# Kernel tuning notes

Hardware: AMD Instinct MI355X
Metric: run time of the kernel (lower is better)

Reference implementation:

```python
import jax, jax.numpy as jnp
import numpy as np

N_CELLS, N_GENES = 10000, 4000
CELL_F, GENE_F = 2000, 50
HID, LAT, NCLUST = 256, 64, 20
N_EDGES = 640000
ALPHA = 1.0


def _lin(key, fan_in, fan_out):
    k1, k2 = jax.random.split(key)
    bound = 1.0 / np.sqrt(fan_in)
    w = jax.random.uniform(k1, (fan_in, fan_out), jnp.float32, -bound, bound)
    b = jax.random.uniform(k2, (fan_out,), jnp.float32, -bound, bound)
    return w, b


def setup_inputs() -> dict:
    key = jax.random.key(0)
    ks = jax.random.split(key, 20)
    inp = {
        'cell_x': jax.random.normal(ks[0], (N_CELLS, CELL_F), jnp.float32),
        'gene_x': jax.random.normal(ks[1], (N_GENES, GENE_F), jnp.float32),
        'edge_row': jax.random.randint(ks[2], (N_EDGES,), 0, N_CELLS),
        'edge_col': jax.random.randint(ks[3], (N_EDGES,), 0, N_GENES),
        'edge_val': jax.random.uniform(ks[4], (N_EDGES,), jnp.float32),
    }
    # layer 0: cell_in=CELL_F, gene_in=GENE_F -> HID
    inp['l0_cs_w'], inp['l0_cs_b'] = _lin(ks[5], CELL_F, HID)
    inp['l0_cn_w'], inp['l0_cn_b'] = _lin(ks[6], GENE_F, HID)
    inp['l0_gs_w'], inp['l0_gs_b'] = _lin(ks[7], GENE_F, HID)
    inp['l0_gn_w'], inp['l0_gn_b'] = _lin(ks[8], CELL_F, HID)
    # layer 1: HID -> HID
    inp['l1_cs_w'], inp['l1_cs_b'] = _lin(ks[9], HID, HID)
    inp['l1_cn_w'], inp['l1_cn_b'] = _lin(ks[10], HID, HID)
    inp['l1_gs_w'], inp['l1_gs_b'] = _lin(ks[11], HID, HID)
    inp['l1_gn_w'], inp['l1_gn_b'] = _lin(ks[12], HID, HID)
    # latent heads and decoders
    inp['cl_w'], inp['cl_b'] = _lin(ks[13], HID, LAT)
    inp['gl_w'], inp['gl_b'] = _lin(ks[14], HID, LAT)
    inp['cd_w'], inp['cd_b'] = _lin(ks[15], LAT, N_GENES)
    inp['gd_w'], inp['gd_b'] = _lin(ks[16], LAT, N_CELLS)
    inp['centers'] = jax.random.normal(ks[17], (NCLUST, LAT), jnp.float32)
    return inp


def _bip_conv(cell_x, gene_x, er, ec, ev,
              cs_w, cs_b, cn_w, cn_b, gs_w, gs_b, gn_w, gn_b):
    # sparse adjacency matmul as gather + segment_sum over edge list
    cell_neigh = jax.ops.segment_sum(ev[:, None] * gene_x[ec], er,
                                     num_segments=cell_x.shape[0])
    gene_neigh = jax.ops.segment_sum(ev[:, None] * cell_x[er], ec,
                                     num_segments=gene_x.shape[0])
    cell_out = jax.nn.relu(cell_x @ cs_w + cs_b + cell_neigh @ cn_w + cn_b)
    gene_out = jax.nn.relu(gene_x @ gs_w + gs_b + gene_neigh @ gn_w + gn_b)
    return cell_out, gene_out


def reference(cell_x, gene_x, edge_row, edge_col, edge_val,
              l0_cs_w, l0_cs_b, l0_cn_w, l0_cn_b, l0_gs_w, l0_gs_b, l0_gn_w, l0_gn_b,
              l1_cs_w, l1_cs_b, l1_cn_w, l1_cn_b, l1_gs_w, l1_gs_b, l1_gn_w, l1_gn_b,
              cl_w, cl_b, gl_w, gl_b, cd_w, cd_b, gd_w, gd_b, centers):
    c, g = _bip_conv(cell_x, gene_x, edge_row, edge_col, edge_val,
                     l0_cs_w, l0_cs_b, l0_cn_w, l0_cn_b,
                     l0_gs_w, l0_gs_b, l0_gn_w, l0_gn_b)
    c, g = _bip_conv(c, g, edge_row, edge_col, edge_val,
                     l1_cs_w, l1_cs_b, l1_cn_w, l1_cn_b,
                     l1_gs_w, l1_gs_b, l1_gn_w, l1_gn_b)
    z_cells = c @ cl_w + cl_b
    z_genes = g @ gl_w + gl_b
    cell_recon = z_cells @ cd_w + cd_b
    gene_recon = z_genes @ gd_w + gd_b
    # Student-t cluster assignment (DEC)
    sq_dist = jnp.sum((z_cells[:, None, :] - centers[None, :, :]) ** 2, axis=-1)
    numerator = (1.0 + sq_dist / ALPHA) ** (-(ALPHA + 1.0) / 2.0)
    q = numerator / jnp.sum(numerator, axis=1, keepdims=True)
    return z_cells, z_genes, cell_recon, gene_recon, q
```

## Files before the change

### kernel.cpp

```cpp
#include <hip/hip_runtime.h>

#define N_CELLS 10000
#define N_GENES 4000
#define CELL_F  2000
#define CELL_FP 2048
#define GENE_F  50
#define GENE_FP 64
#define HID     256
#define LAT     64
#define NCLUST  20
#define N_EDGES 640000

typedef __attribute__((ext_vector_type(8))) short    bf16x8;
typedef __attribute__((ext_vector_type(8))) unsigned short u16x8;
typedef __attribute__((ext_vector_type(4))) float    f32x4;

__device__ __forceinline__ unsigned short f2bf(float f) {
    unsigned int u = __float_as_uint(f);
    unsigned int r = (u + 0x7FFFu + ((u >> 16) & 1u)) >> 16;
    return (unsigned short)r;
}
__device__ __forceinline__ float bf2f(unsigned short h) {
    return __uint_as_float(((unsigned int)h) << 16);
}

#define GLOAD_LDS16(gp, lp) __builtin_amdgcn_global_load_lds( \
    (const __attribute__((address_space(1))) void*)(gp), \
    (__attribute__((address_space(3))) void*)(lp), 16, 0, 0)

struct GemmDesc {
    const unsigned short *A, *BT;
    const float *bias;
    float *C;
    unsigned short *Cbf;
    int M, N, K;
    int gx, nwg, blk0;
};
struct GemmArgs2 { GemmDesc d[2]; };
struct ScatArgs {
    const int *er, *ec; const float *ev;
    int *cur_c, *cur_g;
    int *ci; float *cv; int *gi; float *gv;
};

template<int TM, bool BIAS, bool WF32, bool WBF, bool TEPI, bool QTAIL, bool SCAT>
__global__ __launch_bounds__(256)
void gemm_multi(GemmArgs2 ga, int gemm0, int qstart,
                const float* __restrict__ zq, const float* __restrict__ cent,
                float* __restrict__ qout, ScatArgs sa)
{
    constexpr int SMEM = (TM * 128 + 8192) > 16640 ? (TM * 128 + 8192) : 16640;
    __shared__ __align__(16) unsigned char smem[SMEM];
    unsigned short* As = (unsigned short*)smem;
    unsigned short* Bs = As + TM * 64;

    if (SCAT && (int)blockIdx.x < gemm0) {
        int e = blockIdx.x * 256 + threadIdx.x;
        int r = sa.er[e], c = sa.ec[e];
        float v = sa.ev[e];
        int pc = atomicAdd(&sa.cur_c[r], 1);
        sa.ci[pc] = c; sa.cv[pc] = v;
        int pg = atomicAdd(&sa.cur_g[c], 1);
        sa.gi[pg] = r; sa.gv[pg] = v;
        return;
    }

    if (QTAIL && (int)blockIdx.x >= qstart) {
        float* cs = (float*)smem;
        int tid = threadIdx.x;
        for (int l = tid; l < NCLUST * LAT; l += 256) cs[l] = cent[l];
        __syncthreads();
        int c = (blockIdx.x - qstart) * 256 + tid;
        if (c >= N_CELLS) return;
        float zr[LAT];
        #pragma unroll
        for (int k = 0; k < LAT; ++k) zr[k] = zq[(size_t)c * LAT + k];
        float num[NCLUST];
        float denom = 0.0f;
        for (int j = 0; j < NCLUST; ++j) {
            float d = 0.0f;
            #pragma unroll
            for (int k = 0; k < LAT; ++k) {
                float t = zr[k] - cs[j * LAT + k];
                d += t * t;
            }
            float n = 1.0f / (1.0f + d);
            num[j] = n;
            denom += n;
        }
        float inv = 1.0f / denom;
        for (int j = 0; j < NCLUST; ++j) qout[(size_t)c * NCLUST + j] = num[j] * inv;
        return;
    }

    int b = blockIdx.x;
    int p = (b >= ga.d[1].blk0) ? 1 : 0;
    const GemmDesc d = ga.d[p];
    int lin = b - d.blk0;
    int q8 = d.nwg >> 3, r8 = d.nwg & 7;
    int xcd = lin & 7, idx = lin >> 3;
    int wgid = (xcd < r8 ? xcd * (q8 + 1) : r8 * (q8 + 1) + (xcd - r8) * q8) + idx;
    int by = wgid / d.gx;
    int bx = wgid - by * d.gx;

    const int tid  = threadIdx.x;
    const int lane = tid & 63;
    const int w    = tid >> 6;
    const int cn   = lane & 15;
    const int rj   = lane >> 4;
    const int row0 = by * TM;
    const int col0 = bx * 64;

    constexpr int AI = TM / 32;
    constexpr int MF = TM / 64;

    size_t arow[AI];
    unsigned short* ldsA[AI];
    #pragma unroll
    for (int j = 0; j < AI; ++j) {
        int slot = (w * AI + j) * 64 + lane;
        int rs = slot >> 3, ss = slot & 7, cs = ss ^ (rs & 7);
        arow[j] = (size_t)min(row0 + rs, d.M - 1) * d.K + cs * 8;
        ldsA[j] = As + (w * AI + j) * 512;
    }
    const int sb0 = (w * 2) * 64 + lane;
    const int sb1 = sb0 + 64;
    const int rb0 = sb0 >> 3, cb0 = (sb0 & 7) ^ (rb0 & 7);
    const int rb1 = sb1 >> 3, cb1 = (sb1 & 7) ^ (rb1 & 7);
    const size_t brow0 = (size_t)(col0 + rb0) * d.K + cb0 * 8;
    const size_t brow1 = (size_t)(col0 + rb1) * d.K + cb1 * 8;
    unsigned short* ldsB = Bs + (w * 2) * 512;

    int aoff0[MF], aoff1[MF];
    #pragma unroll
    for (int mf = 0; mf < MF; ++mf) {
        int rA = w * (TM / 4) + mf * 16 + cn, swA = rA & 7, abase = rA * 64;
        aoff0[mf] = abase + ((rj)     ^ swA) * 8;
        aoff1[mf] = abase + ((rj + 4) ^ swA) * 8;
    }

    f32x4 acc[MF][4] = {};

    for (int kt = 0; kt < d.K; kt += 64) {
        #pragma unroll
        for (int j = 0; j < AI; ++j) GLOAD_LDS16(d.A + arow[j] + kt, ldsA[j]);
        GLOAD_LDS16(d.BT + brow0 + kt, ldsB);
        GLOAD_LDS16(d.BT + brow1 + kt, ldsB + 512);
        __syncthreads();
        bf16x8 a0[MF], a1[MF];
        #pragma unroll
        for (int mf = 0; mf < MF; ++mf) {
            a0[mf] = *(const bf16x8*)&As[aoff0[mf]];
            a1[mf] = *(const bf16x8*)&As[aoff1[mf]];
        }
        #pragma unroll
        for (int f = 0; f < 4; ++f) {
            int rB = f * 16 + cn, swB = rB & 7, bb = rB * 64;
            bf16x8 b0 = *(const bf16x8*)&Bs[bb + ((rj)     ^ swB) * 8];
            bf16x8 b1 = *(const bf16x8*)&Bs[bb + ((rj + 4) ^ swB) * 8];
            #pragma unroll
            for (int mf = 0; mf < MF; ++mf) {
                acc[mf][f] = __builtin_amdgcn_mfma_f32_16x16x32_bf16(a0[mf], b0, acc[mf][f], 0, 0, 0);
                acc[mf][f] = __builtin_amdgcn_mfma_f32_16x16x32_bf16(a1[mf], b1, acc[mf][f], 0, 0, 0);
            }
        }
        __syncthreads();
    }

    if (TEPI) {
        float* Cs = (float*)smem;
        __syncthreads();
        #pragma unroll
        for (int f = 0; f < 4; ++f)
            #pragma unroll
            for (int j = 0; j < 4; ++j)
                Cs[(w * 16 + rj * 4 + j) * 65 + f * 16 + cn] = acc[0][f][j];
        __syncthreads();
        #pragma unroll
        for (int i = 0; i < 4; ++i) {
            int slot = tid + i * 256;
            int rr = slot >> 4, c4 = (slot & 15) * 4;
            int gr = row0 + rr, gc = col0 + c4;
            if (gr < d.M && gc < d.N) {
                const float* cp = &Cs[rr * 65 + c4];
                float4 bv = BIAS ? *(const float4*)&d.bias[gc] : float4{0, 0, 0, 0};
                float4 v;
                v.x = cp[0] + bv.x; v.y = cp[1] + bv.y;
                v.z = cp[2] + bv.z; v.w = cp[3] + bv.w;
                *(float4*)&d.C[(size_t)gr * d.N + gc] = v;
            }
        }
    } else {
        #pragma unroll
        for (int mf = 0; mf < MF; ++mf) {
            #pragma unroll
            for (int f = 0; f < 4; ++f) {
                int col = col0 + f * 16 + cn;
                if (col >= d.N) continue;
                float bv = BIAS ? d.bias[col] : 0.0f;
                #pragma unroll
                for (int j = 0; j < 4; ++j) {
                    int r = row0 + w * (TM / 4) + mf * 16 + rj * 4 + j;
                    if (r < d.M) {
                        float val = acc[mf][f][j] + bv;
                        if (WF32) d.C[(size_t)r * d.N + col] = val;
                        if (WBF)  d.Cbf[(size_t)r * d.N + col] = f2bf(val);
                    }
                }
            }
        }
    }
}

struct PackDesc {
    const float* W1; const float* W2; unsigned short* BT;
    int Kr, Kp, N1, N2, Np, xb, blk0;
};
struct PackArgs { PackDesc d[8]; };

#define CNT_BLK   2500
#define CVTC_BLK  10000
#define CVTG_BLK  125
#define PACK_BLK0 (CNT_BLK + CVTC_BLK + CVTG_BLK)

__global__ __launch_bounds__(256)
void prep_kernel(const int* __restrict__ er, const int* __restrict__ ec,
                 int* __restrict__ cnt_c, int* __restrict__ cnt_g,
                 const float* __restrict__ cell_x, unsigned short* __restrict__ cellx_bf,
                 const float* __restrict__ gene_x, unsigned short* __restrict__ genex_bf,
                 PackArgs pa)
{
    __shared__ float tile[32][33];
    int b = blockIdx.x;
    int tid = threadIdx.x;
    if (b < CNT_BLK) {
        int e = b * 256 + tid;
        atomicAdd(&cnt_c[er[e]], 1);
        atomicAdd(&cnt_g[ec[e]], 1);
        return;
    }
    if (b < CNT_BLK + CVTC_BLK) {
        int row = b - CNT_BLK;
        int col = tid * 8;
        u16x8 v = {0, 0, 0, 0, 0, 0, 0, 0};
        if (col < CELL_F) {
            const float* src = cell_x + (size_t)row * CELL_F + col;
            float4 f0 = *(const float4*)src;
            float4 f1 = *(const float4*)(src + 4);
            v[0] = f2bf(f0.x); v[1] = f2bf(f0.y); v[2] = f2bf(f0.z); v[3] = f2bf(f0.w);
            v[4] = f2bf(f1.x); v[5] = f2bf(f1.y); v[6] = f2bf(f1.z); v[7] = f2bf(f1.w);
        }
        ((u16x8*)(cellx_bf + (size_t)row * CELL_FP))[tid] = v;
        return;
    }
    if (b < PACK_BLK0) {
        int idx = (b - CNT_BLK - CVTC_BLK) * 256 + tid;
        int row = idx >> 3, c8 = idx & 7;
        int col = c8 * 8;
        u16x8 v = {0, 0, 0, 0, 0, 0, 0, 0};
        #pragma unroll
        for (int j = 0; j < 8; ++j)
            if (col + j < GENE_F) v[j] = f2bf(gene_x[(size_t)row * GENE_F + col + j]);
        ((u16x8*)(genex_bf + (size_t)row * GENE_FP))[c8] = v;
        return;
    }
    int pb = b;
    int p = 0;
    #pragma unroll
    for (int i = 1; i < 8; ++i) if (pb >= pa.d[i].blk0) p = i;
    const PackDesc d = pa.d[p];
    int local = pb - d.blk0;
    int kb = local % d.xb, nb = local / d.xb;
    int k0 = kb * 32, n0 = nb * 32;
    int tx = tid & 31, ty = tid >> 5;
    #pragma unroll
    for (int yy = 0; yy < 4; ++yy) {
        int k = k0 + ty + yy * 8;
        int n = n0 + tx;
        float v = 0.0f;
        if (k < d.Kr) {
            if (n < d.N1) v = d.W1[(size_t)k * d.N1 + n];
            else if (n < d.N1 + d.N2) v = d.W2[(size_t)k * d.N2 + (n - d.N1)];
        }
        tile[ty + yy * 8][tx] = v;
    }
    __syncthreads();
    #pragma unroll
    for (int yy = 0; yy < 4; ++yy) {
        int n = n0 + ty + yy * 8;
        int k = k0 + tx;
        if (n < d.Np)
            d.BT[(size_t)n * d.Kp + k] = f2bf(tile[tx][ty + yy * 8]);
    }
}

__global__ __launch_bounds__(1024)
void scan2_kernel(const int* __restrict__ cnt_c, int* __restrict__ ptr_c, int* __restrict__ cur_c,
                  const int* __restrict__ cnt_g, int* __restrict__ ptr_g, int* __restrict__ cur_g)
{
    const int* cnt = blockIdx.x ? cnt_g : cnt_c;
    int* ptr = blockIdx.x ? ptr_g : ptr_c;
    int* cur = blockIdx.x ? cur_g : cur_c;
    int  n   = blockIdx.x ? N_GENES : N_CELLS;
    __shared__ int part[1024];
    int t = threadIdx.x;
    int chunk = (n + 1023) / 1024;
    int lo = t * chunk, hi = min(lo + chunk, n);
    int s = 0;
    for (int i = lo; i < hi; ++i) s += cnt[i];
    part[t] = s;
    __syncthreads();
    #pragma unroll
    for (int off = 1; off < 1024; off <<= 1) {
        int v = (t >= off) ? part[t - off] : 0;
        __syncthreads();
        part[t] += v;
        __syncthreads();
    }
    if (t == 1023) ptr[n] = part[1023];
    int run = part[t] - s;
    for (int i = lo; i < hi; ++i) { ptr[i] = run; cur[i] = run; run += cnt[i]; }
}

struct AggSide {
    const int *ptr, *nbr; const float *val;
    const unsigned short *src, *pre;
    const float *b1, *b2;
    unsigned short *out;
};
struct AggArgs { AggSide s[2]; };

__global__ __launch_bounds__(256)
void agg2_kernel(AggArgs aa)
{
    __shared__ __align__(16) float red[4][256];
    int b = blockIdx.x;
    int side = (b >= N_CELLS) ? 1 : 0;
    const AggSide S = aa.s[side];
    int r = side ? b - N_CELLS : b;
    int t = threadIdx.x;
    int w = t >> 6;
    int lane = t & 63;
    int s = S.ptr[r], e = S.ptr[r + 1];
    int n = e - s;
    int chunk = (n + 3) >> 2;
    int ws = s + w * chunk;
    int we = min(ws + chunk, e);
    const ushort4* src4 = (const ushort4*)S.src;
    float4 acc = {0.0f, 0.0f, 0.0f, 0.0f};
    for (int base = ws; base < we; base += 16) {
        int   nb = 0;
        float vb = 0.0f;
        if (lane < 16 && base + lane < we) {
            nb = S.nbr[base + lane];
            vb = S.val[base + lane];
        }
        #pragma unroll
        for (int j = 0; j < 16; ++j) {
            int   jj = __shfl(nb, j);
            float vv = __shfl(vb, j);
            ushort4 a = src4[(size_t)jj * 128 + 64 + lane];
            acc.x += vv * bf2f(a.x);
            acc.y += vv * bf2f(a.y);
            acc.z += vv * bf2f(a.z);
            acc.w += vv * bf2f(a.w);
        }
    }
    *(float4*)&red[w][lane * 4] = acc;
    __syncthreads();
    float x = red[0][t] + red[1][t] + red[2][t] + red[3][t]
            + bf2f(S.pre[(size_t)r * 512 + t]) + S.b1[t] + S.b2[t];
    S.out[(size_t)r * 256 + t] = f2bf(fmaxf(x, 0.0f));
}

extern "C" void kernel_launch(void* const* d_in, const int* in_sizes, int n_in,
                              void* d_out, int out_size, void* d_ws, size_t ws_size,
                              hipStream_t stream)
{
    const float* cell_x  = (const float*)d_in[0];
    const float* gene_x  = (const float*)d_in[1];
    const int*   er      = (const int*)d_in[2];
    const int*   ec      = (const int*)d_in[3];
    const float* ev      = (const float*)d_in[4];
    const float* l0_cs_w = (const float*)d_in[5];  const float* l0_cs_b = (const float*)d_in[6];
    const float* l0_cn_w = (const float*)d_in[7];  const float* l0_cn_b = (const float*)d_in[8];
    const float* l0_gs_w = (const float*)d_in[9];  const float* l0_gs_b = (const float*)d_in[10];
    const float* l0_gn_w = (const float*)d_in[11]; const float* l0_gn_b = (const float*)d_in[12];
    const float* l1_cs_w = (const float*)d_in[13]; const float* l1_cs_b = (const float*)d_in[14];
    const float* l1_cn_w = (const float*)d_in[15]; const float* l1_cn_b = (const float*)d_in[16];
    const float* l1_gs_w = (const float*)d_in[17]; const float* l1_gs_b = (const float*)d_in[18];
    const float* l1_gn_w = (const float*)d_in[19]; const float* l1_gn_b = (const float*)d_in[20];
    const float* cl_w = (const float*)d_in[21]; const float* cl_b = (const float*)d_in[22];
    const float* gl_w = (const float*)d_in[23]; const float* gl_b = (const float*)d_in[24];
    const float* cd_w = (const float*)d_in[25]; const float* cd_b = (const float*)d_in[26];
    const float* gd_w = (const float*)d_in[27]; const float* gd_b = (const float*)d_in[28];
    const float* centers = (const float*)d_in[29];

    float* out = (float*)d_out;
    float* z_cells    = out;
    float* z_genes    = out + 640000;
    float* cell_recon = out + 896000;
    float* gene_recon = out + 40896000;
    float* q          = out + 80896000;

    char* wsp = (char*)d_ws;
    auto alloc = [&](size_t bytes) -> void* {
        void* p = (void*)wsp;
        wsp += (bytes + 255) & ~(size_t)255;
        return p;
    };
    unsigned short* pre_c_bf = (unsigned short*)alloc((size_t)N_CELLS * 512 * 2);
    unsigned short* pre_g_bf = (unsigned short*)alloc((size_t)N_GENES * 512 * 2);
    unsigned short* c1_bf    = (unsigned short*)alloc((size_t)N_CELLS * 256 * 2);
    unsigned short* g1_bf    = (unsigned short*)alloc((size_t)N_GENES * 256 * 2);
    unsigned short* c2_bf    = (unsigned short*)alloc((size_t)N_CELLS * 256 * 2);
    unsigned short* g2_bf    = (unsigned short*)alloc((size_t)N_GENES * 256 * 2);
    unsigned short* zc_bf    = (unsigned short*)alloc((size_t)N_CELLS * 64 * 2);
    unsigned short* zg_bf    = (unsigned short*)alloc((size_t)N_GENES * 64 * 2);
    unsigned short* cellx_bf = (unsigned short*)alloc((size_t)N_CELLS * CELL_FP * 2);
    unsigned short* genex_bf = (unsigned short*)alloc((size_t)N_GENES * GENE_FP * 2);
    unsigned short* W0cT = (unsigned short*)alloc((size_t)512 * CELL_FP * 2);
    unsigned short* W0gT = (unsigned short*)alloc((size_t)512 * GENE_FP * 2);
    unsigned short* W1cT = (unsigned short*)alloc((size_t)512 * HID * 2);
    unsigned short* W1gT = (unsigned short*)alloc((size_t)512 * HID * 2);
    unsigned short* WzcT = (unsigned short*)alloc((size_t)64 * HID * 2);
    unsigned short* WzgT = (unsigned short*)alloc((size_t)64 * HID * 2);
    unsigned short* WdcT = (unsigned short*)alloc((size_t)4032 * 64 * 2);
    unsigned short* WdgT = (unsigned short*)alloc((size_t)10048 * 64 * 2);
    int* cnt_c = (int*)alloc((size_t)(N_CELLS + N_GENES) * 4);
    int* cnt_g = cnt_c + N_CELLS;
    int* ptr_c = (int*)alloc((size_t)(N_CELLS + 1) * 4);
    int* ptr_g = (int*)alloc((size_t)(N_GENES + 1) * 4);
    int* cur_c = (int*)alloc((size_t)N_CELLS * 4);
    int* cur_g = (int*)alloc((size_t)N_GENES * 4);
    int*   ci = (int*)alloc((size_t)N_EDGES * 4);
    float* cv = (float*)alloc((size_t)N_EDGES * 4);
    int*   gi = (int*)alloc((size_t)N_EDGES * 4);
    float* gv = (float*)alloc((size_t)N_EDGES * 4);

    hipMemsetAsync(cnt_c, 0, (size_t)(N_CELLS + N_GENES) * 4, stream);

    {
        PackArgs pa;
        auto set = [&](int i, const float* W1, const float* W2, unsigned short* BT,
                       int Kr, int Kp, int N1, int N2, int Np, int blk0) -> int {
            int xb = Kp / 32, yb = Np / 32;
            pa.d[i] = {W1, W2, BT, Kr, Kp, N1, N2, Np, xb, blk0};
            return blk0 + xb * yb;
        };
        int nb = PACK_BLK0;
        nb = set(0, l0_cs_w, l0_gn_w, W0cT, CELL_F, CELL_FP, HID, HID, 512, nb);
        nb = set(1, l0_gs_w, l0_cn_w, W0gT, GENE_F, GENE_FP, HID, HID, 512, nb);
        nb = set(2, l1_cs_w, l1_gn_w, W1cT, HID, HID, HID, HID, 512, nb);
        nb = set(3, l1_gs_w, l1_cn_w, W1gT, HID, HID, HID, HID, 512, nb);
        nb = set(4, cl_w, nullptr, WzcT, HID, HID, LAT, 0, 64, nb);
        nb = set(5, gl_w, nullptr, WzgT, HID, HID, LAT, 0, 64, nb);
        nb = set(6, cd_w, nullptr, WdcT, LAT, LAT, N_GENES, 0, 4032, nb);
        nb = set(7, gd_w, nullptr, WdgT, LAT, LAT, N_CELLS, 0, 10048, nb);
        prep_kernel<<<nb, 256, 0, stream>>>(er, ec, cnt_c, cnt_g,
                                            cell_x, cellx_bf, gene_x, genex_bf, pa);
    }

    scan2_kernel<<<2, 1024, 0, stream>>>(cnt_c, ptr_c, cur_c, cnt_g, ptr_g, cur_g);

    auto mkdesc = [](const unsigned short* A, const unsigned short* BT, const float* bias,
                     float* C, unsigned short* Cbf, int M, int N, int K, int TMv,
                     int blk0) -> GemmDesc {
        int gx = (N + 63) / 64, gy = (M + TMv - 1) / TMv;
        return {A, BT, bias, C, Cbf, M, N, K, gx, gx * gy, blk0};
    };
    ScatArgs sa0 = {er, ec, ev, cur_c, cur_g, ci, cv, gi, gv};
    ScatArgs saN = {};

    {
        GemmArgs2 ga;
        ga.d[0] = mkdesc(cellx_bf, W0cT, nullptr, nullptr, pre_c_bf, N_CELLS, 512, CELL_FP, 128, CNT_BLK);
        ga.d[1] = mkdesc(genex_bf, W0gT, nullptr, nullptr, pre_g_bf, N_GENES, 512, GENE_FP, 128,
                         CNT_BLK + ga.d[0].nwg);
        gemm_multi<128, false, false, true, false, false, true>
            <<<ga.d[1].blk0 + ga.d[1].nwg, 256, 0, stream>>>(
            ga, CNT_BLK, 1 << 30, nullptr, nullptr, nullptr, sa0);
    }

    {
        AggArgs aa;
        aa.s[0] = {ptr_c, ci, cv, pre_g_bf, pre_c_bf, l0_cs_b, l0_cn_b, c1_bf};
        aa.s[1] = {ptr_g, gi, gv, pre_c_bf, pre_g_bf, l0_gs_b, l0_gn_b, g1_bf};
        agg2_kernel<<<N_CELLS + N_GENES, 256, 0, stream>>>(aa);
    }

    {
        GemmArgs2 ga;
        ga.d[0] = mkdesc(c1_bf, W1cT, nullptr, nullptr, pre_c_bf, N_CELLS, 512, HID, 128, 0);
        ga.d[1] = mkdesc(g1_bf, W1gT, nullptr, nullptr, pre_g_bf, N_GENES, 512, HID, 128,
                         ga.d[0].nwg);
        gemm_multi<128, false, false, true, false, false, false>
            <<<ga.d[1].blk0 + ga.d[1].nwg, 256, 0, stream>>>(
            ga, 0, 1 << 30, nullptr, nullptr, nullptr, saN);
    }

    {
        AggArgs aa;
        aa.s[0] = {ptr_c, ci, cv, pre_g_bf, pre_c_bf, l1_cs_b, l1_cn_b, c2_bf};
        aa.s[1] = {ptr_g, gi, gv, pre_c_bf, pre_g_bf, l1_gs_b, l1_gn_b, g2_bf};
        agg2_kernel<<<N_CELLS + N_GENES, 256, 0, stream>>>(aa);
    }

    {
        GemmArgs2 ga;
        ga.d[0] = mkdesc(c2_bf, WzcT, cl_b, z_cells, zc_bf, N_CELLS, LAT, HID, 64, 0);
        ga.d[1] = mkdesc(g2_bf, WzgT, gl_b, z_genes, zg_bf, N_GENES, LAT, HID, 64, ga.d[0].nwg);
        gemm_multi<64, true, true, true, false, false, false>
            <<<ga.d[1].blk0 + ga.d[1].nwg, 256, 0, stream>>>(
            ga, 0, 1 << 30, nullptr, nullptr, nullptr, saN);
    }

    {
        GemmArgs2 ga;
        ga.d[0] = mkdesc(zc_bf, WdcT, cd_b, cell_recon, nullptr, N_CELLS, N_GENES, LAT, 64, 0);
        ga.d[1] = mkdesc(zg_bf, WdgT, gd_b, gene_recon, nullptr, N_GENES, N_CELLS, LAT, 64,
                         ga.d[0].nwg);
        int qstart = ga.d[1].blk0 + ga.d[1].nwg;
        int qblocks = (N_CELLS + 255) / 256;
        gemm_multi<64, true, true, false, true, true, false>
            <<<qstart + qblocks, 256, 0, stream>>>(
            ga, 0, qstart, z_cells, centers, q, saN);
    }
}
```

Measured before the change: 480.2 us.

## Gather raw gene features into cell rows and fuse layer-0 cell aggregation into GEMM

Layer 0's cell-neighbor term is reassociated: the sparse sum of raw 50-wide gene features is gathered into an extra K-segment of the padded cell input, and the l0_cn weights are appended to the packed cell weight. This lets one big GEMM produce the final relu'd cell output with both biases, and drops the 256-wide cell-side aggregation pass for layer 0. The gene side only computes its self term from gene features, and the cell GEMM's second half supplies the gene-neighbor projection. The cost is a larger K (2112), one extra gather kernel, and an extra launch that serialises the first GEMM stage.

```diff
diff --git a/kernel.cpp b/kernel.cpp
--- a/kernel.cpp
+++ b/kernel.cpp
@@ -3,7 +3,7 @@
 #define N_CELLS 10000
 #define N_GENES 4000
 #define CELL_F  2000
-#define CELL_FP 2048
+#define CELL_FX 2112
 #define GENE_F  50
 #define GENE_FP 64
 #define HID     256
@@ -35,6 +35,8 @@
     unsigned short *Cbf;
     int M, N, K;
     int gx, nwg, blk0;
+    const float *bias2;
+    unsigned short *Cbf2;
 };
 struct GemmArgs2 { GemmDesc d[2]; };
 struct ScatArgs {
@@ -43,7 +45,7 @@
     int *ci; float *cv; int *gi; float *gv;
 };
 
-template<int TM, bool BIAS, bool WF32, bool WBF, bool TEPI, bool QTAIL, bool SCAT>
+template<int TM, bool BIAS, bool WF32, bool WBF, bool TEPI, bool QTAIL, bool SCAT, bool RSPLIT>
 __global__ __launch_bounds__(256)
 void gemm_multi(GemmArgs2 ga, int gemm0, int qstart,
                 const float* __restrict__ zq, const float* __restrict__ cent,
@@ -188,6 +190,27 @@
                 v.x = cp[0] + bv.x; v.y = cp[1] + bv.y;
                 v.z = cp[2] + bv.z; v.w = cp[3] + bv.w;
                 *(float4*)&d.C[(size_t)gr * d.N + gc] = v;
+            }
+        }
+    } else if (RSPLIT) {
+        #pragma unroll
+        for (int mf = 0; mf < MF; ++mf) {
+            #pragma unroll
+            for (int f = 0; f < 4; ++f) {
+                int col = col0 + f * 16 + cn;
+                #pragma unroll
+                for (int j = 0; j < 4; ++j) {
+                    int r = row0 + w * (TM / 4) + mf * 16 + rj * 4 + j;
+                    if (r < d.M) {
+                        float val = acc[mf][f][j];
+                        if (col < 256) {
+                            val += d.bias[col] + d.bias2[col];
+                            d.Cbf[(size_t)r * 256 + col] = f2bf(fmaxf(val, 0.0f));
+                        } else {
+                            d.Cbf2[(size_t)r * 256 + (col - 256)] = f2bf(val);
+                        }
+                    }
+                }
             }
         }
     } else {
@@ -212,8 +235,46 @@
     }
 }
 
+__global__ __launch_bounds__(256)
+void rawgather_kernel(const int* __restrict__ ptr, const int* __restrict__ nbr,
+                      const float* __restrict__ val,
+                      const unsigned short* __restrict__ gx,
+                      unsigned short* __restrict__ cellx)
+{
+    int w = threadIdx.x >> 6, lane = threadIdx.x & 63;
+    int r = blockIdx.x * 4 + w;
+    int s = ptr[r], e = ptr[r + 1];
+    int g = lane >> 4, sub = lane & 15;
+    const ushort4* gx4 = (const ushort4*)gx;
+    float4 acc = {0.0f, 0.0f, 0.0f, 0.0f};
+    for (int base = s; base < e; base += 16) {
+        int nb = 0; float vb = 0.0f;
+        if (lane < 16 && base + lane < e) { nb = nbr[base + lane]; vb = val[base + lane]; }
+        #pragma unroll
+        for (int jj = 0; jj < 4; ++jj) {
+            int ei = jj * 4 + g;
+            int j  = __shfl(nb, ei);
+            float v = __shfl(vb, ei);
+            ushort4 a = gx4[(size_t)j * 16 + sub];
+            acc.x += v * bf2f(a.x);
+            acc.y += v * bf2f(a.y);
+            acc.z += v * bf2f(a.z);
+            acc.w += v * bf2f(a.w);
+        }
+    }
+    acc.x += __shfl_xor(acc.x, 16); acc.x += __shfl_xor(acc.x, 32);
+    acc.y += __shfl_xor(acc.y, 16); acc.y += __shfl_xor(acc.y, 32);
+    acc.z += __shfl_xor(acc.z, 16); acc.z += __shfl_xor(acc.z, 32);
+    acc.w += __shfl_xor(acc.w, 16); acc.w += __shfl_xor(acc.w, 32);
+    if (lane < 16) {
+        ushort4 o;
+        o.x = f2bf(acc.x); o.y = f2bf(acc.y); o.z = f2bf(acc.z); o.w = f2bf(acc.w);
+        ((ushort4*)(cellx + (size_t)r * CELL_FX + 2048))[sub] = o;
+    }
+}
+
 struct PackDesc {
-    const float* W1; const float* W2; unsigned short* BT;
+    const float* W1; const float* W2; const float* W3; unsigned short* BT;
     int Kr, Kp, N1, N2, Np, xb, blk0;
 };
 struct PackArgs { PackDesc d[8]; };
@@ -250,7 +311,7 @@
             v[0] = f2bf(f0.x); v[1] = f2bf(f0.y); v[2] = f2bf(f0.z); v[3] = f2bf(f0.w);
             v[4] = f2bf(f1.x); v[5] = f2bf(f1.y); v[6] = f2bf(f1.z); v[7] = f2bf(f1.w);
         }
-        ((u16x8*)(cellx_bf + (size_t)row * CELL_FP))[tid] = v;
+        ((u16x8*)(cellx_bf + (size_t)row * CELL_FX))[tid] = v;
         return;
     }
     if (b < PACK_BLK0) {
@@ -281,6 +342,9 @@
         if (k < d.Kr) {
             if (n < d.N1) v = d.W1[(size_t)k * d.N1 + n];
             else if (n < d.N1 + d.N2) v = d.W2[(size_t)k * d.N2 + (n - d.N1)];
+        } else if (d.W3 && k >= 2048) {
+            int kk = k - 2048;
+            if (kk < GENE_F && n < HID) v = d.W3[(size_t)kk * HID + n];
         }
         tile[ty + yy * 8][tx] = v;
     }
@@ -327,17 +391,18 @@
     const unsigned short *src, *pre;
     const float *b1, *b2;
     unsigned short *out;
+    int srcRow4, srcOff4, preRow;
 };
-struct AggArgs { AggSide s[2]; };
+struct AggArgs { AggSide s[2]; int nc; };
 
 __global__ __launch_bounds__(256)
 void agg2_kernel(AggArgs aa)
 {
     __shared__ __align__(16) float red[4][256];
     int b = blockIdx.x;
-    int side = (b >= N_CELLS) ? 1 : 0;
+    int side = (b >= aa.nc) ? 1 : 0;
     const AggSide S = aa.s[side];
-    int r = side ? b - N_CELLS : b;
+    int r = side ? b - aa.nc : b;
     int t = threadIdx.x;
     int w = t >> 6;
     int lane = t & 63;
@@ -359,7 +424,7 @@
         for (int j = 0; j < 16; ++j) {
             int   jj = __shfl(nb, j);
             float vv = __shfl(vb, j);
-            ushort4 a = src4[(size_t)jj * 128 + 64 + lane];
+            ushort4 a = src4[(size_t)jj * S.srcRow4 + S.srcOff4 + lane];
             acc.x += vv * bf2f(a.x);
             acc.y += vv * bf2f(a.y);
             acc.z += vv * bf2f(a.z);
@@ -369,7 +434,7 @@
     *(float4*)&red[w][lane * 4] = acc;
     __syncthreads();
     float x = red[0][t] + red[1][t] + red[2][t] + red[3][t]
-            + bf2f(S.pre[(size_t)r * 512 + t]) + S.b1[t] + S.b2[t];
+            + bf2f(S.pre[(size_t)r * S.preRow + t]) + S.b1[t] + S.b2[t];
     S.out[(size_t)r * 256 + t] = f2bf(fmaxf(x, 0.0f));
 }
 
@@ -417,10 +482,10 @@
     unsigned short* g2_bf    = (unsigned short*)alloc((size_t)N_GENES * 256 * 2);
     unsigned short* zc_bf    = (unsigned short*)alloc((size_t)N_CELLS * 64 * 2);
     unsigned short* zg_bf    = (unsigned short*)alloc((size_t)N_GENES * 64 * 2);
-    unsigned short* cellx_bf = (unsigned short*)alloc((size_t)N_CELLS * CELL_FP * 2);
+    unsigned short* cellx_bf = (unsigned short*)alloc((size_t)N_CELLS * CELL_FX * 2);
     unsigned short* genex_bf = (unsigned short*)alloc((size_t)N_GENES * GENE_FP * 2);
-    unsigned short* W0cT = (unsigned short*)alloc((size_t)512 * CELL_FP * 2);
-    unsigned short* W0gT = (unsigned short*)alloc((size_t)512 * GENE_FP * 2);
+    unsigned short* W0cT = (unsigned short*)alloc((size_t)512 * CELL_FX * 2);
+    unsigned short* W0gT = (unsigned short*)alloc((size_t)256 * GENE_FP * 2);
     unsigned short* W1cT = (unsigned short*)alloc((size_t)512 * HID * 2);
     unsigned short* W1gT = (unsigned short*)alloc((size_t)512 * HID * 2);
     unsigned short* WzcT = (unsigned short*)alloc((size_t)64 * HID * 2);
@@ -437,26 +502,29 @@
     float* cv = (float*)alloc((size_t)N_EDGES * 4);
     int*   gi = (int*)alloc((size_t)N_EDGES * 4);
     float* gv = (float*)alloc((size_t)N_EDGES * 4);
+    unsigned short* pre_cgn_bf = c2_bf;
+    unsigned short* pre_gs_bf  = g2_bf;
 
     hipMemsetAsync(cnt_c, 0, (size_t)(N_CELLS + N_GENES) * 4, stream);
 
     {
         PackArgs pa;
-        auto set = [&](int i, const float* W1, const float* W2, unsigned short* BT,
-                       int Kr, int Kp, int N1, int N2, int Np, int blk0) -> int {
+        auto set = [&](int i, const float* W1, const float* W2, const float* W3,
+                       unsigned short* BT, int Kr, int Kp, int N1, int N2, int Np,
+                       int blk0) -> int {
             int xb = Kp / 32, yb = Np / 32;
-            pa.d[i] = {W1, W2, BT, Kr, Kp, N1, N2, Np, xb, blk0};
+            pa.d[i] = {W1, W2, W3, BT, Kr, Kp, N1, N2, Np, xb, blk0};
             return blk0 + xb * yb;
         };
         int nb = PACK_BLK0;
-        nb = set(0, l0_cs_w, l0_gn_w, W0cT, CELL_F, CELL_FP, HID, HID, 512, nb);
-        nb = set(1, l0_gs_w, l0_cn_w, W0gT, GENE_F, GENE_FP, HID, HID, 512, nb);
-        nb = set(2, l1_cs_w, l1_gn_w, W1cT, HID, HID, HID, HID, 512, nb);
-        nb = set(3, l1_gs_w, l1_cn_w, W1gT, HID, HID, HID, HID, 512, nb);
-        nb = set(4, cl_w, nullptr, WzcT, HID, HID, LAT, 0, 64, nb);
-        nb = set(5, gl_w, nullptr, WzgT, HID, HID, LAT, 0, 64, nb);
-        nb = set(6, cd_w, nullptr, WdcT, LAT, LAT, N_GENES, 0, 4032, nb);
-        nb = set(7, gd_w, nullptr, WdgT, LAT, LAT, N_CELLS, 0, 10048, nb);
+        nb = set(0, l0_cs_w, l0_gn_w, l0_cn_w, W0cT, CELL_F, CELL_FX, HID, HID, 512, nb);
+        nb = set(1, l0_gs_w, nullptr, nullptr, W0gT, GENE_F, GENE_FP, HID, 0, 256, nb);
+        nb = set(2, l1_cs_w, l1_gn_w, nullptr, W1cT, HID, HID, HID, HID, 512, nb);
+        nb = set(3, l1_gs_w, l1_cn_w, nullptr, W1gT, HID, HID, HID, HID, 512, nb);
+        nb = set(4, cl_w, nullptr, nullptr, WzcT, HID, HID, LAT, 0, 64, nb);
+        nb = set(5, gl_w, nullptr, nullptr, WzgT, HID, HID, LAT, 0, 64, nb);
+        nb = set(6, cd_w, nullptr, nullptr, WdcT, LAT, LAT, N_GENES, 0, 4032, nb);
+        nb = set(7, gd_w, nullptr, nullptr, WdgT, LAT, LAT, N_CELLS, 0, 10048, nb);
         prep_kernel<<<nb, 256, 0, stream>>>(er, ec, cnt_c, cnt_g,
                                             cell_x, cellx_bf, gene_x, genex_bf, pa);
     }
@@ -467,26 +535,39 @@
                      float* C, unsigned short* Cbf, int M, int N, int K, int TMv,
                      int blk0) -> GemmDesc {
         int gx = (N + 63) / 64, gy = (M + TMv - 1) / TMv;
-        return {A, BT, bias, C, Cbf, M, N, K, gx, gx * gy, blk0};
+        return {A, BT, bias, C, Cbf, M, N, K, gx, gx * gy, blk0, nullptr, nullptr};
     };
     ScatArgs sa0 = {er, ec, ev, cur_c, cur_g, ci, cv, gi, gv};
     ScatArgs saN = {};
 
     {
         GemmArgs2 ga;
-        ga.d[0] = mkdesc(cellx_bf, W0cT, nullptr, nullptr, pre_c_bf, N_CELLS, 512, CELL_FP, 128, CNT_BLK);
-        ga.d[1] = mkdesc(genex_bf, W0gT, nullptr, nullptr, pre_g_bf, N_GENES, 512, GENE_FP, 128,
-                         CNT_BLK + ga.d[0].nwg);
-        gemm_multi<128, false, false, true, false, false, true>
-            <<<ga.d[1].blk0 + ga.d[1].nwg, 256, 0, stream>>>(
+        ga.d[0] = mkdesc(genex_bf, W0gT, nullptr, nullptr, pre_gs_bf, N_GENES, 256, GENE_FP, 128, CNT_BLK);
+        ga.d[1] = ga.d[0]; ga.d[1].blk0 = 1 << 30;
+        gemm_multi<128, false, false, true, false, false, true, false>
+            <<<CNT_BLK + ga.d[0].nwg, 256, 0, stream>>>(
             ga, CNT_BLK, 1 << 30, nullptr, nullptr, nullptr, sa0);
     }
 
+    rawgather_kernel<<<N_CELLS / 4, 256, 0, stream>>>(ptr_c, ci, cv, genex_bf, cellx_bf);
+
+    {
+        GemmArgs2 ga;
+        ga.d[0] = mkdesc(cellx_bf, W0cT, l0_cs_b, nullptr, c1_bf, N_CELLS, 512, CELL_FX, 128, 0);
+        ga.d[0].bias2 = l0_cn_b;
+        ga.d[0].Cbf2  = pre_cgn_bf;
+        ga.d[1] = ga.d[0]; ga.d[1].blk0 = 1 << 30;
+        gemm_multi<128, false, false, false, false, false, false, true>
+            <<<ga.d[0].nwg, 256, 0, stream>>>(
+            ga, 0, 1 << 30, nullptr, nullptr, nullptr, saN);
+    }
+
     {
         AggArgs aa;
-        aa.s[0] = {ptr_c, ci, cv, pre_g_bf, pre_c_bf, l0_cs_b, l0_cn_b, c1_bf};
-        aa.s[1] = {ptr_g, gi, gv, pre_c_bf, pre_g_bf, l0_gs_b, l0_gn_b, g1_bf};
-        agg2_kernel<<<N_CELLS + N_GENES, 256, 0, stream>>>(aa);
+        aa.nc = 0;
+        aa.s[1] = {ptr_g, gi, gv, pre_cgn_bf, pre_gs_bf, l0_gs_b, l0_gn_b, g1_bf, 64, 0, 256};
+        aa.s[0] = aa.s[1];
+        agg2_kernel<<<N_GENES, 256, 0, stream>>>(aa);
     }
 
     {
@@ -494,15 +575,16 @@
         ga.d[0] = mkdesc(c1_bf, W1cT, nullptr, nullptr, pre_c_bf, N_CELLS, 512, HID, 128, 0);
         ga.d[1] = mkdesc(g1_bf, W1gT, nullptr, nullptr, pre_g_bf, N_GENES, 512, HID, 128,
                          ga.d[0].nwg);
-        gemm_multi<128, false, false, true, false, false, false>
+        gemm_multi<128, false, false, true, false, false, false, false>
             <<<ga.d[1].blk0 + ga.d[1].nwg, 256, 0, stream>>>(
             ga, 0, 1 << 30, nullptr, nullptr, nullptr, saN);
     }
 
     {
         AggArgs aa;
-        aa.s[0] = {ptr_c, ci, cv, pre_g_bf, pre_c_bf, l1_cs_b, l1_cn_b, c2_bf};
-        aa.s[1] = {ptr_g, gi, gv, pre_c_bf, pre_g_bf, l1_gs_b, l1_gn_b, g2_bf};
+        aa.nc = N_CELLS;
+        aa.s[0] = {ptr_c, ci, cv, pre_g_bf, pre_c_bf, l1_cs_b, l1_cn_b, c2_bf, 128, 64, 512};
+        aa.s[1] = {ptr_g, gi, gv, pre_c_bf, pre_g_bf, l1_gs_b, l1_gn_b, g2_bf, 128, 64, 512};
         agg2_kernel<<<N_CELLS + N_GENES, 256, 0, stream>>>(aa);
     }
 
@@ -510,7 +592,7 @@
         GemmArgs2 ga;
         ga.d[0] = mkdesc(c2_bf, WzcT, cl_b, z_cells, zc_bf, N_CELLS, LAT, HID, 64, 0);
         ga.d[1] = mkdesc(g2_bf, WzgT, gl_b, z_genes, zg_bf, N_GENES, LAT, HID, 64, ga.d[0].nwg);
-        gemm_multi<64, true, true, true, false, false, false>
+        gemm_multi<64, true, true, true, false, false, false, false>
             <<<ga.d[1].blk0 + ga.d[1].nwg, 256, 0, stream>>>(
             ga, 0, 1 << 30, nullptr, nullptr, nullptr, saN);
     }
@@ -522,7 +604,7 @@
                          ga.d[0].nwg);
         int qstart = ga.d[1].blk0 + ga.d[1].nwg;
         int qblocks = (N_CELLS + 255) / 256;
-        gemm_multi<64, true, true, false, true, true, false>
+        gemm_multi<64, true, true, false, true, true, false, false>
             <<<qstart + qblocks, 256, 0, stream>>>(
             ga, 0, qstart, z_cells, centers, q, saN);
     }
```

After: 436.4 us. 1.1x faster.
